# Kernel optimization log

Measured on AMD Instinct MI355X. Metric: run time of the kernel, lower is better.

Reference implementation:

```python
import jax, jax.numpy as jnp
import numpy as np

N_NODES = 100000
N_EDGES = 1600000
IN_CH = 128
HID = 64
HEADS = 2
OUT_CH = 2
EDGE_DIM = 3
NEG_SLOPE = 0.2
EPS = 1e-16  # PyG softmax denominator epsilon


def gat_conv(x, edge_index, edge_attr, W, We, att_src, att_dst, att_edge, bias, heads, out_ch, concat):
    """Faithful PyG GATConv (edge_dim enabled, eval mode, add_self_loops handled by caller=False here
    since the repo passes raw edge_index; PyG default add_self_loops=True is intentionally mirrored below)."""
    N = x.shape[0]
    src, dst = edge_index[0], edge_index[1]
    H, C = heads, out_ch
    h = (x @ W).reshape(N, H, C)                    # [N,H,C] node projections
    e = (edge_attr @ We).reshape(-1, H, C)          # [E,H,C] edge projections
    a_src = jnp.sum(h * att_src, axis=-1)           # [N,H]
    a_dst = jnp.sum(h * att_dst, axis=-1)           # [N,H]
    alpha = a_src[src] + a_dst[dst] + jnp.sum(e * att_edge, axis=-1)  # [E,H]
    alpha = jax.nn.leaky_relu(alpha, NEG_SLOPE)
    # segment softmax over incoming edges of each dst node
    amax = jax.ops.segment_max(alpha, dst, num_segments=N)            # [N,H]
    amax = jnp.where(jnp.isfinite(amax), amax, 0.0)
    alpha = jnp.exp(alpha - amax[dst])
    denom = jax.ops.segment_sum(alpha, dst, num_segments=N)           # [N,H]
    alpha = alpha / (denom[dst] + EPS)
    msg = h[src] * alpha[:, :, None]                                  # [E,H,C]
    out = jax.ops.segment_sum(msg, dst, num_segments=N)               # [N,H,C]
    if concat:
        out = out.reshape(N, H * C)
    else:
        out = out.mean(axis=1)
    return out + bias


def add_self_loops(edge_index, edge_attr, n):
    loops = jnp.arange(n, dtype=edge_index.dtype)
    ei = jnp.concatenate([edge_index, jnp.stack([loops, loops])], axis=1)
    ea = jnp.concatenate([edge_attr, jnp.zeros((n, edge_attr.shape[1]), edge_attr.dtype)], axis=0)
    return ei, ea


def setup_inputs() -> dict:
    key = jax.random.key(0)
    ks = jax.random.split(key, 16)
    s = 0.1
    x = jax.random.normal(ks[0], (N_NODES, IN_CH), jnp.float32)
    edge_index = jax.random.randint(ks[1], (2, N_EDGES), 0, N_NODES, jnp.int64 if jax.config.jax_enable_x64 else jnp.int32)
    edge_feat = jax.random.normal(ks[2], (N_EDGES, EDGE_DIM), jnp.float32)
    HC = HEADS * HID
    return {
        "x": x, "edge_index": edge_index, "edge_feat": edge_feat,
        "W1": jax.random.normal(ks[3], (IN_CH, HC), jnp.float32) * s,
        "We1": jax.random.normal(ks[4], (EDGE_DIM, HC), jnp.float32) * s,
        "as1": jax.random.normal(ks[5], (1, HEADS, HID), jnp.float32) * s,
        "ad1": jax.random.normal(ks[6], (1, HEADS, HID), jnp.float32) * s,
        "ae1": jax.random.normal(ks[7], (1, HEADS, HID), jnp.float32) * s,
        "b1": jnp.zeros((HC,), jnp.float32),
        "W2": jax.random.normal(ks[8], (HC, OUT_CH), jnp.float32) * s,
        "We2": jax.random.normal(ks[9], (EDGE_DIM, OUT_CH), jnp.float32) * s,
        "as2": jax.random.normal(ks[10], (1, 1, OUT_CH), jnp.float32) * s,
        "ad2": jax.random.normal(ks[11], (1, 1, OUT_CH), jnp.float32) * s,
        "ae2": jax.random.normal(ks[12], (1, 1, OUT_CH), jnp.float32) * s,
        "b2": jnp.zeros((OUT_CH,), jnp.float32),
    }


def reference(x, edge_index, edge_feat, W1, We1, as1, ad1, ae1, b1, W2, We2, as2, ad2, ae2, b2):
    # eval mode: F.dropout is identity
    ei, ea = add_self_loops(edge_index, edge_feat, x.shape[0])  # PyG GATConv default add_self_loops=True
    h = gat_conv(x, ei, ea, W1, We1, as1, ad1, ae1, b1, HEADS, HID, concat=True)
    h = jax.nn.elu(h)
    out = gat_conv(h, ei, ea, W2, We2, as2, ad2, ae2, b2, 1, OUT_CH, concat=False)
    return out
```

## Files before the change

### kernel.cpp

```cpp
#include <hip/hip_runtime.h>
#include <hip/hip_bf16.h>

#define NN 100000
#define NE 1600000
#define NEG_SLOPE 0.2f
#define GEPS 1e-16f
#define WSHIFT 4.0f

typedef __attribute__((ext_vector_type(8))) short short8;
typedef __attribute__((ext_vector_type(4))) float f32x4;
typedef __attribute__((ext_vector_type(2))) _Float16 h2v;

__device__ __forceinline__ unsigned short f2b(float f) {
  unsigned u = __float_as_uint(f);
  u += 0x7fffu + ((u >> 16) & 1u);
  return (unsigned short)(u >> 16);
}
__device__ __forceinline__ unsigned short f2h(float f) {
  _Float16 h = (_Float16)f;
  return __builtin_bit_cast(unsigned short, h);
}
__device__ __forceinline__ unsigned pkh2(float lo, float hi) {
  return (unsigned)f2h(lo) | ((unsigned)f2h(hi) << 16);
}
__device__ __forceinline__ float dot2h(unsigned a, unsigned b, float c) {
  return __builtin_amdgcn_fdot2(__builtin_bit_cast(h2v, a), __builtin_bit_cast(h2v, b), c, false);
}
__device__ __forceinline__ unsigned permb(unsigned s0, unsigned s1, int sel) {
  return __builtin_amdgcn_perm(s0, s1, sel);
}
#define HSEL_LO 0x05040100
#define HSEL_HI 0x07060302
#define ONE2    0x3C003C00u

__global__ void k_prep(const float* __restrict__ We1, const float* __restrict__ ae1,
                       const float* __restrict__ We2, const float* __restrict__ ae2,
                       const float* __restrict__ W1, const float* __restrict__ as1,
                       const float* __restrict__ ad1,
                       float* __restrict__ q, float4* __restrict__ pq) {
  int t = threadIdx.x;
  if (t < 6) {
    int d = t >> 1, hh = t & 1;
    float s = 0.f;
    for (int c = 0; c < 64; ++c) s += We1[d * 128 + hh * 64 + c] * ae1[hh * 64 + c];
    q[t] = s;
  } else if (t < 9) {
    int d = t - 6;
    q[8 + d] = We2[d * 2 + 0] * ae2[0] + We2[d * 2 + 1] * ae2[1];
  }
  if (t < 128) {
    float s0 = 0.f, s1 = 0.f, d0 = 0.f, d1 = 0.f;
    for (int c = 0; c < 64; ++c) {
      float w0 = W1[t * 128 + c], w1 = W1[t * 128 + 64 + c];
      s0 += w0 * as1[c];      s1 += w1 * as1[64 + c];
      d0 += w0 * ad1[c];      d1 += w1 * ad1[64 + c];
    }
    pq[t] = make_float4(s0, s1, d0, d1);
  }
}

__global__ __launch_bounds__(512, 4) void k_gemm(const float* __restrict__ x,
                                                 const float* __restrict__ W,
                                                 const float4* __restrict__ pq,
                                                 unsigned short* __restrict__ h1b,
                                                 float* __restrict__ a1s,
                                                 float* __restrict__ a1d) {
  __shared__ unsigned short xa[128 * 128];
  __shared__ unsigned short wt[128 * 128];
  int t = threadIdx.x;
  int row0 = blockIdx.x * 128;

  {
    int kr = t >> 2, n0 = (t & 3) * 32;
    const float* wp = &W[kr * 128 + n0];
    int cb = kr >> 3, klo = kr & 7;
#pragma unroll
    for (int j = 0; j < 8; ++j) {
      float4 v = *(const float4*)&wp[j * 4];
      int n = n0 + j * 4;
      wt[(n + 0) * 128 + ((cb ^ ((n + 0) & 15)) * 8) + klo] = f2b(v.x);
      wt[(n + 1) * 128 + ((cb ^ ((n + 1) & 15)) * 8) + klo] = f2b(v.y);
      wt[(n + 2) * 128 + ((cb ^ ((n + 2) & 15)) * 8) + klo] = f2b(v.z);
      wt[(n + 3) * 128 + ((cb ^ ((n + 3) & 15)) * 8) + klo] = f2b(v.w);
    }
  }
  {
    int lrow = t >> 2, qq = t & 3;
    int grow = row0 + lrow; if (grow >= NN) grow = NN - 1;
    const float* xp = &x[(size_t)grow * 128 + qq * 32];
    const float4* pqp = &pq[qq * 32];
    float ps0 = 0.f, ps1 = 0.f, pd0 = 0.f, pd1 = 0.f;
    int sw = lrow & 15;
#pragma unroll
    for (int j = 0; j < 4; ++j) {
      float4 u = *(const float4*)&xp[j * 8];
      float4 v = *(const float4*)&xp[j * 8 + 4];
      float xs[8] = {u.x, u.y, u.z, u.w, v.x, v.y, v.z, v.w};
      short8 sv;
#pragma unroll
      for (int e = 0; e < 8; ++e) {
        float4 pv = pqp[j * 8 + e];
        ps0 += xs[e] * pv.x; ps1 += xs[e] * pv.y;
        pd0 += xs[e] * pv.z; pd1 += xs[e] * pv.w;
        sv[e] = (short)f2b(xs[e]);
      }
      int c = qq * 4 + j;
      *(short8*)&xa[lrow * 128 + ((c ^ sw) * 8)] = sv;
    }
    ps0 += __shfl_xor(ps0, 1); ps0 += __shfl_xor(ps0, 2);
    ps1 += __shfl_xor(ps1, 1); ps1 += __shfl_xor(ps1, 2);
    pd0 += __shfl_xor(pd0, 1); pd0 += __shfl_xor(pd0, 2);
    pd1 += __shfl_xor(pd1, 1); pd1 += __shfl_xor(pd1, 2);
    if (qq == 0) {
      *(float2*)&a1s[grow * 2] = make_float2(ps0, ps1);
      *(float2*)&a1d[grow * 2] = make_float2(pd0, pd1);
    }
  }
  __syncthreads();

  int lane = t & 63, w = t >> 6;
  int m = lane & 15, quad = lane >> 4;
  int wm = (w & 1) * 64, wn = (w >> 1) * 32;
  f32x4 acc[4][2];
#pragma unroll
  for (int mi = 0; mi < 4; ++mi)
#pragma unroll
    for (int ni = 0; ni < 2; ++ni) acc[mi][ni] = (f32x4)(0.f);

#pragma unroll
  for (int kk = 0; kk < 4; ++kk) {
    int c = kk * 4 + quad;
    int co = (c ^ m) * 8;
    short8 a[4], b[2];
#pragma unroll
    for (int mi = 0; mi < 4; ++mi)
      a[mi] = *(const short8*)&xa[(wm + mi * 16 + m) * 128 + co];
#pragma unroll
    for (int ni = 0; ni < 2; ++ni)
      b[ni] = *(const short8*)&wt[(wn + ni * 16 + m) * 128 + co];
#pragma unroll
    for (int mi = 0; mi < 4; ++mi)
#pragma unroll
      for (int ni = 0; ni < 2; ++ni)
        acc[mi][ni] = __builtin_amdgcn_mfma_f32_16x16x32_bf16(a[mi], b[ni], acc[mi][ni], 0, 0, 0);
  }
#pragma unroll
  for (int mi = 0; mi < 4; ++mi)
#pragma unroll
    for (int r = 0; r < 4; ++r) {
      int grow = row0 + wm + mi * 16 + quad * 4 + r;
      if (grow >= NN) grow = NN - 1;
#pragma unroll
      for (int ni = 0; ni < 2; ++ni)
        h1b[(size_t)grow * 128 + wn + ni * 16 + m] = f2h(acc[mi][ni][r]);
    }
}

__global__ void k_hist(const int* __restrict__ ei, int* __restrict__ deg,
                       int* __restrict__ rank) {
  int t4 = blockIdx.x * 256 + threadIdx.x;
  if (t4 >= NE / 4) return;
  int4 d = *(const int4*)&ei[NE + t4 * 4];
  int4 rk;
  rk.x = atomicAdd(&deg[d.x], 1);
  rk.y = atomicAdd(&deg[d.y], 1);
  rk.z = atomicAdd(&deg[d.z], 1);
  rk.w = atomicAdd(&deg[d.w], 1);
  *(int4*)&rank[t4 * 4] = rk;
}

__device__ __forceinline__ int padlen(int d) { return (d + 8) & ~7; }

__global__ void k_scan1(const int* __restrict__ deg, int* __restrict__ bsum) {
  __shared__ int lds[256];
  int t = threadIdx.x;
  int base = blockIdx.x * 1024 + t * 4;
  int s = 0;
  for (int j = 0; j < 4; ++j) { int i = base + j; s += (i < NN) ? padlen(deg[i]) : 0; }
  lds[t] = s; __syncthreads();
  for (int o = 128; o > 0; o >>= 1) { if (t < o) lds[t] += lds[t + o]; __syncthreads(); }
  if (t == 0) bsum[blockIdx.x] = lds[0];
}

__global__ void k_scan2(int* __restrict__ bsum, int nb) {
  __shared__ int lds[128];
  int t = threadIdx.x;
  int v = (t < nb) ? bsum[t] : 0;
  lds[t] = v; __syncthreads();
  for (int o = 1; o < 128; o <<= 1) {
    int u = (t >= o) ? lds[t - o] : 0;
    __syncthreads();
    lds[t] += u;
    __syncthreads();
  }
  if (t < nb) bsum[t] = lds[t] - v;
}

__global__ void k_scan3(const int* __restrict__ deg, const int* __restrict__ bbase,
                        const float* __restrict__ a1s, const float* __restrict__ a1d,
                        int* __restrict__ rowptr, float4* __restrict__ cpk) {
  __shared__ int lds[256];
  int t = threadIdx.x;
  int base = blockIdx.x * 1024 + t * 4;
  int v[4]; int s = 0;
  for (int j = 0; j < 4; ++j) { int i = base + j; v[j] = (i < NN) ? padlen(deg[i]) : 0; s += v[j]; }
  lds[t] = s; __syncthreads();
  for (int o = 1; o < 256; o <<= 1) {
    int u = (t >= o) ? lds[t - o] : 0;
    __syncthreads();
    lds[t] += u;
    __syncthreads();
  }
  int excl = lds[t] - s + bbase[blockIdx.x];
  for (int j = 0; j < 4; ++j) {
    int i = base + j;
    if (i <= NN) rowptr[i] = excl;
    if (i < NN) {
      float al0 = a1s[i * 2] + a1d[i * 2];
      float al1 = a1s[i * 2 + 1] + a1d[i * 2 + 1];
      al0 = al0 > 0.f ? al0 : NEG_SLOPE * al0;
      al1 = al1 > 0.f ? al1 : NEG_SLOPE * al1;
      float4 pk;
      pk.x = __uint_as_float(pkh2(__expf(al0 - WSHIFT), __expf(al1 - WSHIFT)));
      pk.y = 0.f; pk.z = __int_as_float(i); pk.w = 0.f;
      cpk[excl] = pk;
      float4 pad;
      pad.x = 0.f; pad.y = -1e30f; pad.z = __int_as_float(i); pad.w = 0.f;
      for (int k = 1 + deg[i]; k < v[j]; ++k) cpk[excl + k] = pad;
    }
    excl += v[j];
  }
}

__global__ void k_scatter(const int* __restrict__ ei, const float* __restrict__ ef,
                          const float* __restrict__ a1s, const float* __restrict__ a1d,
                          const float* __restrict__ q, const int* __restrict__ rowptr,
                          const int* __restrict__ rank, float4* __restrict__ cpk) {
  int t4 = blockIdx.x * 256 + threadIdx.x;
  if (t4 >= NE / 4) return;
  int e0 = t4 * 4;
  int4 ss = *(const int4*)&ei[e0];
  int4 dd = *(const int4*)&ei[NE + e0];
  int4 rk = *(const int4*)&rank[e0];
  float4 fA = *(const float4*)&ef[e0 * 3];
  float4 fB = *(const float4*)&ef[e0 * 3 + 4];
  float4 fC = *(const float4*)&ef[e0 * 3 + 8];
  float f[4][3] = {{fA.x, fA.y, fA.z}, {fA.w, fB.x, fB.y},
                   {fB.z, fB.w, fC.x}, {fC.y, fC.z, fC.w}};
  int src[4] = {ss.x, ss.y, ss.z, ss.w};
  int dst[4] = {dd.x, dd.y, dd.z, dd.w};
  int rnk[4] = {rk.x, rk.y, rk.z, rk.w};
#pragma unroll
  for (int j = 0; j < 4; ++j) {
    float e0h = f[j][0] * q[0] + f[j][1] * q[2] + f[j][2] * q[4];
    float e1h = f[j][0] * q[1] + f[j][1] * q[3] + f[j][2] * q[5];
    float ez  = f[j][0] * q[8] + f[j][1] * q[9] + f[j][2] * q[10];
    float al0 = a1s[src[j] * 2] + a1d[dst[j] * 2] + e0h;
    float al1 = a1s[src[j] * 2 + 1] + a1d[dst[j] * 2 + 1] + e1h;
    al0 = al0 > 0.f ? al0 : NEG_SLOPE * al0;
    al1 = al1 > 0.f ? al1 : NEG_SLOPE * al1;
    int pos = rowptr[dst[j]] + 1 + rnk[j];
    float4 pk;
    pk.x = __uint_as_float(pkh2(__expf(al0 - WSHIFT), __expf(al1 - WSHIFT)));
    pk.y = ez; pk.z = __int_as_float(src[j]); pk.w = 0.f;
    cpk[pos] = pk;
  }
}

__global__ __launch_bounds__(256) void k_agg1(const unsigned short* __restrict__ h1b,
                                              const int* __restrict__ rowptr,
                                              const float4* __restrict__ cpk,
                                              const float* __restrict__ b1,
                                              const float* __restrict__ W2,
                                              const float* __restrict__ as2,
                                              const float* __restrict__ ad2,
                                              float4* __restrict__ nd) {
  int n = (int)((blockIdx.x * 256 + threadIdx.x) >> 6);
  int lane = threadIdx.x & 63;
  if (n >= NN) return;
  int s0 = rowptr[n], s1 = rowptr[n + 1];
  int g = lane >> 4;
  int lp = lane & 15;
  int wsel = (lp >= 8) ? HSEL_HI : HSEL_LO;

  float acc[8];
#pragma unroll
  for (int j = 0; j < 8; ++j) acc[j] = 0.f;
  float den = 0.f;

  int i = s0;
  for (; i + 16 <= s1; i += 16) {
    float4 pA = cpk[i + g], pB = cpk[i + 4 + g], pC = cpk[i + 8 + g], pD = cpk[i + 12 + g];
    uint4 vA = *((const uint4*)(h1b + ((size_t)__float_as_int(pA.z) << 7)) + lp);
    uint4 vB = *((const uint4*)(h1b + ((size_t)__float_as_int(pB.z) << 7)) + lp);
    uint4 vC = *((const uint4*)(h1b + ((size_t)__float_as_int(pC.z) << 7)) + lp);
    uint4 vD = *((const uint4*)(h1b + ((size_t)__float_as_int(pD.z) << 7)) + lp);
    unsigned wAB = permb(__float_as_uint(pB.x), __float_as_uint(pA.x), wsel);
    unsigned wCD = permb(__float_as_uint(pD.x), __float_as_uint(pC.x), wsel);
    den = dot2h(wAB, ONE2, den);
    den = dot2h(wCD, ONE2, den);
    acc[0] = dot2h(permb(vB.x, vA.x, HSEL_LO), wAB, acc[0]);
    acc[1] = dot2h(permb(vB.x, vA.x, HSEL_HI), wAB, acc[1]);
    acc[2] = dot2h(permb(vB.y, vA.y, HSEL_LO), wAB, acc[2]);
    acc[3] = dot2h(permb(vB.y, vA.y, HSEL_HI), wAB, acc[3]);
    acc[4] = dot2h(permb(vB.z, vA.z, HSEL_LO), wAB, acc[4]);
    acc[5] = dot2h(permb(vB.z, vA.z, HSEL_HI), wAB, acc[5]);
    acc[6] = dot2h(permb(vB.w, vA.w, HSEL_LO), wAB, acc[6]);
    acc[7] = dot2h(permb(vB.w, vA.w, HSEL_HI), wAB, acc[7]);
    acc[0] = dot2h(permb(vD.x, vC.x, HSEL_LO), wCD, acc[0]);
    acc[1] = dot2h(permb(vD.x, vC.x, HSEL_HI), wCD, acc[1]);
    acc[2] = dot2h(permb(vD.y, vC.y, HSEL_LO), wCD, acc[2]);
    acc[3] = dot2h(permb(vD.y, vC.y, HSEL_HI), wCD, acc[3]);
    acc[4] = dot2h(permb(vD.z, vC.z, HSEL_LO), wCD, acc[4]);
    acc[5] = dot2h(permb(vD.z, vC.z, HSEL_HI), wCD, acc[5]);
    acc[6] = dot2h(permb(vD.w, vC.w, HSEL_LO), wCD, acc[6]);
    acc[7] = dot2h(permb(vD.w, vC.w, HSEL_HI), wCD, acc[7]);
  }
  if (i < s1) {
    float4 pA = cpk[i + g], pB = cpk[i + 4 + g];
    uint4 vA = *((const uint4*)(h1b + ((size_t)__float_as_int(pA.z) << 7)) + lp);
    uint4 vB = *((const uint4*)(h1b + ((size_t)__float_as_int(pB.z) << 7)) + lp);
    unsigned wAB = permb(__float_as_uint(pB.x), __float_as_uint(pA.x), wsel);
    den = dot2h(wAB, ONE2, den);
    acc[0] = dot2h(permb(vB.x, vA.x, HSEL_LO), wAB, acc[0]);
    acc[1] = dot2h(permb(vB.x, vA.x, HSEL_HI), wAB, acc[1]);
    acc[2] = dot2h(permb(vB.y, vA.y, HSEL_LO), wAB, acc[2]);
    acc[3] = dot2h(permb(vB.y, vA.y, HSEL_HI), wAB, acc[3]);
    acc[4] = dot2h(permb(vB.z, vA.z, HSEL_LO), wAB, acc[4]);
    acc[5] = dot2h(permb(vB.z, vA.z, HSEL_HI), wAB, acc[5]);
    acc[6] = dot2h(permb(vB.w, vA.w, HSEL_LO), wAB, acc[6]);
    acc[7] = dot2h(permb(vB.w, vA.w, HSEL_HI), wAB, acc[7]);
  }
#pragma unroll
  for (int o = 16; o <= 32; o <<= 1) {
    den += __shfl_xor(den, o);
#pragma unroll
    for (int j = 0; j < 8; ++j) acc[j] += __shfl_xor(acc[j], o);
  }
  float4 bA = *(const float4*)&b1[lp * 8];
  float4 bB = *(const float4*)&b1[lp * 8 + 4];
  float bb[8] = {bA.x, bA.y, bA.z, bA.w, bB.x, bB.y, bB.z, bB.w};
  float inv = 1.f / (den + GEPS);
  float r[8];
#pragma unroll
  for (int j = 0; j < 8; ++j) {
    float v = acc[j] * inv + bb[j];
    r[j] = v > 0.f ? v : __expf(v) - 1.f;
  }
  float4 wA = *(const float4*)&W2[lp * 16];
  float4 wB = *(const float4*)&W2[lp * 16 + 4];
  float4 wC = *(const float4*)&W2[lp * 16 + 8];
  float4 wD = *(const float4*)&W2[lp * 16 + 12];
  float p20 = r[0] * wA.x + r[1] * wA.z + r[2] * wB.x + r[3] * wB.z
            + r[4] * wC.x + r[5] * wC.z + r[6] * wD.x + r[7] * wD.z;
  float p21 = r[0] * wA.y + r[1] * wA.w + r[2] * wB.y + r[3] * wB.w
            + r[4] * wC.y + r[5] * wC.w + r[6] * wD.y + r[7] * wD.w;
#pragma unroll
  for (int o = 1; o <= 8; o <<= 1) { p20 += __shfl_xor(p20, o); p21 += __shfl_xor(p21, o); }
  if (lane == 0) {
    float4 v;
    v.x = p20; v.y = p21;
    v.z = p20 * as2[0] + p21 * as2[1];
    v.w = p20 * ad2[0] + p21 * ad2[1];
    nd[n] = v;
  }
}

__global__ __launch_bounds__(256) void k_agg2(const int* __restrict__ rowptr,
                                              const float4* __restrict__ cpk,
                                              const float4* __restrict__ nd,
                                              const float* __restrict__ b2,
                                              float* __restrict__ out) {
  int wid = (int)((blockIdx.x * 256 + threadIdx.x) >> 6);
  int lane = threadIdx.x & 63;
  int g = lane >> 4, lp = lane & 15;
  int n = wid * 4 + g;
  if (n >= NN) return;
  int s0 = rowptr[n], s1 = rowptr[n + 1];
  float adn = nd[n].w;
  float den = 0.f, acc0 = 0.f, acc1 = 0.f;
  for (int i = s0 + lp; i < s1; i += 16) {
    float4 pk = cpk[i];
    int s = __float_as_int(pk.z);
    float4 ns = nd[s];
    float v = ns.z + adn + pk.y;
    v = v > 0.f ? v : NEG_SLOPE * v;
    float p = __expf(v);
    den += p;
    acc0 += p * ns.x;
    acc1 += p * ns.y;
  }
#pragma unroll
  for (int o = 1; o <= 8; o <<= 1) {
    den += __shfl_xor(den, o);
    acc0 += __shfl_xor(acc0, o);
    acc1 += __shfl_xor(acc1, o);
  }
  if (lp == 0) {
    float2 r;
    r.x = acc0 / (den + GEPS) + b2[0];
    r.y = acc1 / (den + GEPS) + b2[1];
    *(float2*)&out[n * 2] = r;
  }
}

extern "C" void kernel_launch(void* const* d_in, const int* in_sizes, int n_in,
                              void* d_out, int out_size, void* d_ws, size_t ws_size,
                              hipStream_t stream) {
  (void)in_sizes; (void)n_in; (void)out_size; (void)ws_size;
  const float* x   = (const float*)d_in[0];
  const int*   ei  = (const int*)d_in[1];
  const float* ef  = (const float*)d_in[2];
  const float* W1  = (const float*)d_in[3];
  const float* We1 = (const float*)d_in[4];
  const float* as1 = (const float*)d_in[5];
  const float* ad1 = (const float*)d_in[6];
  const float* ae1 = (const float*)d_in[7];
  const float* b1  = (const float*)d_in[8];
  const float* W2  = (const float*)d_in[9];
  const float* We2 = (const float*)d_in[10];
  const float* as2 = (const float*)d_in[11];
  const float* ad2 = (const float*)d_in[12];
  const float* ae2 = (const float*)d_in[13];
  const float* b2  = (const float*)d_in[14];
  float* out = (float*)d_out;

  char* w = (char*)d_ws;
  auto alloc = [&](size_t bytes) -> char* {
    char* p = w; w += (bytes + 255) & ~(size_t)255; return p;
  };
  unsigned short* h1b = (unsigned short*)alloc((size_t)NN * 128 * 2);
  float*  a1s    = (float*)alloc((size_t)NN * 2 * 4);
  float*  a1d    = (float*)alloc((size_t)NN * 2 * 4);
  float4* nd     = (float4*)alloc((size_t)NN * 16);
  float*  q      = (float*)alloc(64);
  float4* pq     = (float4*)alloc(128 * 16);
  int*    deg    = (int*)alloc((size_t)NN * 4);
  int*    rowptr = (int*)alloc((size_t)(NN + 1) * 4);
  int*    rank   = (int*)alloc((size_t)NE * 4);
  int*    bsum   = (int*)alloc(128 * 4);
  float4* cpk    = (float4*)alloc(((size_t)NE + 8 * NN) * 16);

  const int NB_SCAN = (NN + 1023) / 1024;

  hipLaunchKernelGGL(k_prep, dim3(1), dim3(128), 0, stream,
                     We1, ae1, We2, ae2, W1, as1, ad1, q, pq);
  hipLaunchKernelGGL(k_gemm, dim3((NN + 127) / 128), dim3(512), 0, stream,
                     x, W1, pq, h1b, a1s, a1d);
  hipMemsetAsync(deg, 0, (size_t)NN * 4, stream);
  hipLaunchKernelGGL(k_hist, dim3((NE / 4 + 255) / 256), dim3(256), 0, stream, ei, deg, rank);
  hipLaunchKernelGGL(k_scan1, dim3(NB_SCAN), dim3(256), 0, stream, deg, bsum);
  hipLaunchKernelGGL(k_scan2, dim3(1), dim3(128), 0, stream, bsum, NB_SCAN);
  hipLaunchKernelGGL(k_scan3, dim3(NB_SCAN), dim3(256), 0, stream,
                     deg, bsum, a1s, a1d, rowptr, cpk);
  hipLaunchKernelGGL(k_scatter, dim3((NE / 4 + 255) / 256), dim3(256), 0, stream,
                     ei, ef, a1s, a1d, q, rowptr, rank, cpk);
  hipLaunchKernelGGL(k_agg1, dim3((NN * 64 + 255) / 256), dim3(256), 0, stream,
                     h1b, rowptr, cpk, b1, W2, as2, ad2, nd);
  hipLaunchKernelGGL(k_agg2, dim3(((NN + 3) / 4 * 64 + 255) / 256), dim3(256), 0, stream,
                     rowptr, cpk, nd, b2, out);
}
```

Before: 387.4 us.

## Replace global-atomic degree histogram with LDS-privatized per-chunk 16-bit histograms

The degree histogram now runs in 128 blocks, each covering one edge chunk and one quarter of the node range. Counts go into LDS with packed 16-bit atomics, and ranks are stored as 16-bit values. A new k_sumdeg kernel turns the per-chunk counts into per-chunk offsets and total degrees, and k_scatter adds the chunk offset when computing each edge's position. This removes contended global atomics and halves rank traffic, but each block reads its whole edge chunk four times, the launch has only 128 blocks, and there is an extra kernel plus a 6.4MB offset array.

Measured after the change: 347.8 us. 1.11x faster.

```diff
diff --git a/kernel.cpp b/kernel.cpp
--- a/kernel.cpp
+++ b/kernel.cpp
@@ -6,6 +6,12 @@
 #define NEG_SLOPE 0.2f
 #define GEPS 1e-16f
 #define WSHIFT 4.0f
+
+#define HB 32
+#define EB (NE / HB)
+#define HPASS 4
+#define HBIN 25000
+#define HBW (HBIN / 2)
 
 typedef __attribute__((ext_vector_type(8))) short short8;
 typedef __attribute__((ext_vector_type(4))) float f32x4;
@@ -156,17 +162,47 @@
     }
 }
 
-__global__ void k_hist(const int* __restrict__ ei, int* __restrict__ deg,
-                       int* __restrict__ rank) {
-  int t4 = blockIdx.x * 256 + threadIdx.x;
-  if (t4 >= NE / 4) return;
-  int4 d = *(const int4*)&ei[NE + t4 * 4];
-  int4 rk;
-  rk.x = atomicAdd(&deg[d.x], 1);
-  rk.y = atomicAdd(&deg[d.y], 1);
-  rk.z = atomicAdd(&deg[d.z], 1);
-  rk.w = atomicAdd(&deg[d.w], 1);
-  *(int4*)&rank[t4 * 4] = rk;
+__global__ __launch_bounds__(1024) void k_hist(const int* __restrict__ ei,
+                                               unsigned short* __restrict__ off16,
+                                               unsigned short* __restrict__ rank) {
+  __shared__ unsigned cnt[HBW];
+  int b = blockIdx.x >> 2;
+  int pass = blockIdx.x & 3;
+  int base = pass * HBIN;
+  int t = threadIdx.x;
+  for (int i = t; i < HBW; i += 1024) cnt[i] = 0;
+  __syncthreads();
+  const int* dsts = &ei[NE + b * EB];
+  for (int i = t * 4; i < EB; i += 4096) {
+    int4 d = *(const int4*)&dsts[i];
+    int dv[4] = {d.x, d.y, d.z, d.w};
+#pragma unroll
+    for (int j = 0; j < 4; ++j) {
+      int rel = dv[j] - base;
+      if ((unsigned)rel < (unsigned)HBIN) {
+        unsigned sh = (unsigned)(rel & 1) << 4;
+        unsigned old = atomicAdd(&cnt[rel >> 1], 1u << sh);
+        rank[b * EB + i + j] = (unsigned short)((old >> sh) & 0xffffu);
+      }
+    }
+  }
+  __syncthreads();
+  unsigned short* dp = &off16[(size_t)b * NN + base];
+  for (int i = t; i < HBW; i += 1024) *(unsigned*)&dp[i * 2] = cnt[i];
+}
+
+__global__ void k_sumdeg(unsigned short* __restrict__ off16, int* __restrict__ deg) {
+  int n = blockIdx.x * 256 + threadIdx.x;
+  if (n >= NN) return;
+  int run = 0;
+#pragma unroll
+  for (int b = 0; b < HB; ++b) {
+    size_t idx = (size_t)b * NN + n;
+    int c = off16[idx];
+    off16[idx] = (unsigned short)run;
+    run += c;
+  }
+  deg[n] = run;
 }
 
 __device__ __forceinline__ int padlen(int d) { return (d + 8) & ~7; }
@@ -235,13 +271,17 @@
 __global__ void k_scatter(const int* __restrict__ ei, const float* __restrict__ ef,
                           const float* __restrict__ a1s, const float* __restrict__ a1d,
                           const float* __restrict__ q, const int* __restrict__ rowptr,
-                          const int* __restrict__ rank, float4* __restrict__ cpk) {
+                          const unsigned short* __restrict__ rank,
+                          const unsigned short* __restrict__ off16,
+                          float4* __restrict__ cpk) {
   int t4 = blockIdx.x * 256 + threadIdx.x;
   if (t4 >= NE / 4) return;
   int e0 = t4 * 4;
+  int hb = e0 / EB;
+  const unsigned short* offp = &off16[(size_t)hb * NN];
   int4 ss = *(const int4*)&ei[e0];
   int4 dd = *(const int4*)&ei[NE + e0];
-  int4 rk = *(const int4*)&rank[e0];
+  ushort4 rk = *(const ushort4*)&rank[e0];
   float4 fA = *(const float4*)&ef[e0 * 3];
   float4 fB = *(const float4*)&ef[e0 * 3 + 4];
   float4 fC = *(const float4*)&ef[e0 * 3 + 8];
@@ -259,7 +299,7 @@
     float al1 = a1s[src[j] * 2 + 1] + a1d[dst[j] * 2 + 1] + e1h;
     al0 = al0 > 0.f ? al0 : NEG_SLOPE * al0;
     al1 = al1 > 0.f ? al1 : NEG_SLOPE * al1;
-    int pos = rowptr[dst[j]] + 1 + rnk[j];
+    int pos = rowptr[dst[j]] + 1 + (int)offp[dst[j]] + rnk[j];
     float4 pk;
     pk.x = __uint_as_float(pkh2(__expf(al0 - WSHIFT), __expf(al1 - WSHIFT)));
     pk.y = ez; pk.z = __int_as_float(src[j]); pk.w = 0.f;
@@ -437,7 +477,8 @@
   float4* pq     = (float4*)alloc(128 * 16);
   int*    deg    = (int*)alloc((size_t)NN * 4);
   int*    rowptr = (int*)alloc((size_t)(NN + 1) * 4);
-  int*    rank   = (int*)alloc((size_t)NE * 4);
+  unsigned short* rank  = (unsigned short*)alloc((size_t)NE * 2);
+  unsigned short* off16 = (unsigned short*)alloc((size_t)HB * NN * 2);
   int*    bsum   = (int*)alloc(128 * 4);
   float4* cpk    = (float4*)alloc(((size_t)NE + 8 * NN) * 16);
 
@@ -447,14 +488,14 @@
                      We1, ae1, We2, ae2, W1, as1, ad1, q, pq);
   hipLaunchKernelGGL(k_gemm, dim3((NN + 127) / 128), dim3(512), 0, stream,
                      x, W1, pq, h1b, a1s, a1d);
-  hipMemsetAsync(deg, 0, (size_t)NN * 4, stream);
-  hipLaunchKernelGGL(k_hist, dim3((NE / 4 + 255) / 256), dim3(256), 0, stream, ei, deg, rank);
+  hipLaunchKernelGGL(k_hist, dim3(HB * HPASS), dim3(1024), 0, stream, ei, off16, rank);
+  hipLaunchKernelGGL(k_sumdeg, dim3((NN + 255) / 256), dim3(256), 0, stream, off16, deg);
   hipLaunchKernelGGL(k_scan1, dim3(NB_SCAN), dim3(256), 0, stream, deg, bsum);
   hipLaunchKernelGGL(k_scan2, dim3(1), dim3(128), 0, stream, bsum, NB_SCAN);
   hipLaunchKernelGGL(k_scan3, dim3(NB_SCAN), dim3(256), 0, stream,
                      deg, bsum, a1s, a1d, rowptr, cpk);
   hipLaunchKernelGGL(k_scatter, dim3((NE / 4 + 255) / 256), dim3(256), 0, stream,
-                     ei, ef, a1s, a1d, q, rowptr, rank, cpk);
+                     ei, ef, a1s, a1d, q, rowptr, rank, off16, cpk);
   hipLaunchKernelGGL(k_agg1, dim3((NN * 64 + 255) / 256), dim3(256), 0, stream,
                      h1b, rowptr, cpk, b1, W2, as2, ad2, nd);
   hipLaunchKernelGGL(k_agg2, dim3(((NN + 3) / 4 * 64 + 255) / 256), dim3(256), 0, stream,
```
